# Performance work log

Measured on AMD Instinct MI355X. Metric: run time of the kernel, lower is better.

Reference implementation:

```python
import jax, jax.numpy as jnp
import numpy as np

B, L, D, H = 8, 1024, 1024, 16
DH = D // H  # 64


def setup_inputs() -> dict:
    key = jax.random.key(0)
    ks = jax.random.split(key, 6)
    x = jax.random.normal(ks[0], (B, L, D), dtype=jnp.float32)
    mask = jax.random.randint(ks[1], (1, L, L), 0, 2).astype(jnp.float32)
    # params initialized ~ normal(std=0.1) as in the module's _initialize
    Wk = jax.random.normal(ks[2], (D, D), dtype=jnp.float32) * 0.1
    Wv = jax.random.normal(ks[3], (D, D), dtype=jnp.float32) * 0.1
    Wq = jax.random.normal(ks[4], (D, D), dtype=jnp.float32) * 0.1
    Wo = jax.random.normal(ks[5], (D, D), dtype=jnp.float32) * 0.1
    return {"x": x, "mask": mask, "Wk": Wk, "Wv": Wv, "Wq": Wq, "Wo": Wo}


def reference(x, mask, Wk, Wv, Wq, Wo):
    # torch Linear: y = x @ W.T
    k = jnp.einsum('bld,ed->ble', x, Wk).reshape(B, L, H, DH)
    v = jnp.einsum('bld,ed->ble', x, Wv).reshape(B, L, H, DH)
    q = jnp.einsum('bld,ed->ble', x, Wq).reshape(B, L, H, DH)
    # explicit score matrix [B, H, L, L]
    scores = jnp.einsum('blhe,bmhe->bhlm', q, k)
    m = mask[:, None]  # (1, 1, L, L) broadcasts over batch and heads
    scores = scores * m - 1e9 * (1.0 - m)
    scale = np.float32(1.0 / np.sqrt(DH))
    weights = jax.nn.softmax(scores * scale, axis=-1)
    out = jnp.einsum('bhlm,bmhe->blhe', weights, v).reshape(B, L, D)
    out = jnp.einsum('bld,ed->ble', out, Wo)  # output_linear (n_heads > 1)
    return out
```

## Files before the change

kernel.cpp:

```cpp
#include <hip/hip_runtime.h>

#define B_  8
#define L_  1024
#define D_  1024
#define H_  16
#define DH_ 64

typedef unsigned short u16;
typedef __attribute__((ext_vector_type(8))) short short8;
typedef __attribute__((ext_vector_type(8))) _Float16 half8;
typedef __attribute__((ext_vector_type(4))) float floatx4;
typedef __attribute__((ext_vector_type(16))) float floatx16;

static __device__ __forceinline__ u16 f2bf(float f) {
  union { float f; unsigned u; } cv; cv.f = f;
  unsigned u = cv.u;
  return (u16)((u + 0x7fffu + ((u >> 16) & 1u)) >> 16);
}
static __device__ __forceinline__ u16 f2h(float f) {
  union { _Float16 h; u16 u; } cv; cv.h = (_Float16)f; return cv.u;
}
static __device__ __forceinline__ unsigned pack_bf2(float a, float b) {
  union { float f; unsigned u; } ua, ub; ua.f = a; ub.f = b;
  return __builtin_amdgcn_perm(ub.u + 0x8000u, ua.u + 0x8000u, 0x07060302u);
}

#if __has_builtin(__builtin_amdgcn_exp2f)
#define EXP2(x) __builtin_amdgcn_exp2f(x)
#else
#define EXP2(x) __expf((x) * 0.6931471805599453f)
#endif

__global__ void cast_all(const float* __restrict__ x,  const float* __restrict__ wq,
                         const float* __restrict__ wk, const float* __restrict__ wv,
                         const float* __restrict__ wo, const float* __restrict__ mask,
                         u16* __restrict__ xf,  u16* __restrict__ wqf,
                         u16* __restrict__ wkf, u16* __restrict__ wvf,
                         u16* __restrict__ wof, float* __restrict__ biasP) {
  int blk = blockIdx.x;
  if (blk >= 12288) {
    int i = (blk - 12288) * 256 + threadIdx.x;
    int e = i & 3, lane = (i >> 2) & 63, rr = (i >> 8) & 3, t = (i >> 10) & 1;
    int c = (i >> 11) & 15, w = (i >> 15) & 3, qt = i >> 17;
    int kk  = e + 8 * rr + 4 * (lane >> 5);
    int row = qt * 128 + w * 32 + (lane & 31);
    int key = c * 64 + t * 32 + kk;
    biasP[i] = (mask[(size_t)row * L_ + key] - 1.0f) * 1.8033688e8f - 34.624681f;
    return;
  }
  const float* src; u16* dst; int off;
  if (blk < 8192)       { src = x;  dst = xf;  off = blk; }
  else if (blk < 9216)  { src = wq; dst = wqf; off = blk - 8192; }
  else if (blk < 10240) { src = wk; dst = wkf; off = blk - 9216; }
  else if (blk < 11264) { src = wv; dst = wvf; off = blk - 10240; }
  else                  { src = wo; dst = wof; off = blk - 11264; }
  int i = off * 1024 + threadIdx.x * 4;
  float4 f = *(const float4*)(src + i);
  ushort4 r;
  r.x = f2h(f.x); r.y = f2h(f.y); r.z = f2h(f.z); r.w = f2h(f.w);
  *(ushort4*)(dst + i) = r;
}

typedef __attribute__((address_space(3))) void  lds_void;
typedef const __attribute__((address_space(1))) void g_void;
static __device__ __forceinline__ void load_lds16(const void* g, void* l) {
  __builtin_amdgcn_global_load_lds((g_void*)g, (lds_void*)l, 16, 0, 0);
}

__global__ __launch_bounds__(256) void gemm_qkv(const u16* __restrict__ A,
                                                const u16* __restrict__ wq,
                                                const u16* __restrict__ wk,
                                                const u16* __restrict__ wv,
                                                u16* __restrict__ qf,
                                                u16* __restrict__ kf,
                                                u16* __restrict__ vb) {
  const int K = D_, N = D_;
  int nb = blockIdx.x;
  const u16* Bw; u16* Cp; float scale; int obf;
  if (nb < 8)       { Bw = wq; Cp = qf; scale = 0.18033688f; obf = 0; }
  else if (nb < 16) { Bw = wk; Cp = kf; scale = 1.0f;        obf = 0; }
  else              { Bw = wv; Cp = vb; scale = 1.0f;        obf = 1; }
  const int n0 = (nb & 7) * 128;

  __shared__ u16 lA[2 * 128 * 32];
  __shared__ u16 lB[2 * 128 * 32];
  const int tid  = threadIdx.x;
  const int w    = tid >> 6;
  const int lane = tid & 63;
  const int m    = lane & 15;
  const int kg   = lane >> 4;
  const int m0   = blockIdx.y * 128;
  const int wm   = (w >> 1) * 64;
  const int wn   = (w & 1) * 64;
  const int rowS = tid >> 2;
  const int part = tid & 3;
  const int csrc8 = ((part ^ ((rowS >> 1) & 3))) * 8;
  const int kgs   = (kg ^ ((m >> 1) & 3)) * 8;

  floatx4 acc[4][4];
#pragma unroll
  for (int i = 0; i < 4; ++i)
#pragma unroll
    for (int j = 0; j < 4; ++j)
#pragma unroll
      for (int r = 0; r < 4; ++r) acc[i][j][r] = 0.0f;

  auto STAGE = [&](int k0, int bufsel) {
#pragma unroll
    for (int rnd = 0; rnd < 2; ++rnd) {
      const u16* ga = A  + (size_t)(m0 + rnd * 64 + rowS) * K + k0 + csrc8;
      const u16* gb = Bw + (size_t)(n0 + rnd * 64 + rowS) * K + k0 + csrc8;
      load_lds16(ga, lA + bufsel * 4096 + rnd * 2048 + w * 512);
      load_lds16(gb, lB + bufsel * 4096 + rnd * 2048 + w * 512);
    }
  };

  STAGE(0, 0);
  STAGE(32, 1);

  for (int k0 = 0; k0 < K; k0 += 32) {
    const int buf = (k0 >> 5) & 1;
    if (k0 + 32 < K) { asm volatile("s_waitcnt vmcnt(4)" ::: "memory"); }
    else             { asm volatile("s_waitcnt vmcnt(0)" ::: "memory"); }
    __builtin_amdgcn_s_barrier();
    __builtin_amdgcn_sched_barrier(0);

    const u16* pA = lA + buf * 4096;
    const u16* pB = lB + buf * 4096;
    half8 af[4], bf[4];
#pragma unroll
    for (int i = 0; i < 4; ++i) af[i] = *(const half8*)&pA[(wm + i * 16 + m) * 32 + kgs];
#pragma unroll
    for (int i = 0; i < 4; ++i) bf[i] = *(const half8*)&pB[(wn + i * 16 + m) * 32 + kgs];
#pragma unroll
    for (int mi = 0; mi < 4; ++mi)
#pragma unroll
      for (int ni = 0; ni < 4; ++ni)
        acc[mi][ni] = __builtin_amdgcn_mfma_f32_16x16x32_f16(af[mi], bf[ni], acc[mi][ni], 0, 0, 0);

    __builtin_amdgcn_sched_barrier(0);
    __builtin_amdgcn_s_barrier();
    if (k0 + 64 < K) STAGE(k0 + 64, buf);
  }

#pragma unroll
  for (int mi = 0; mi < 4; ++mi)
#pragma unroll
    for (int ni = 0; ni < 4; ++ni)
#pragma unroll
      for (int r = 0; r < 4; ++r) {
        int row = m0 + wm + mi * 16 + kg * 4 + r;
        int col = n0 + wn + ni * 16 + m;
        size_t idx = (size_t)row * N + col;
        float vv = acc[mi][ni][r] * scale;
        Cp[idx] = obf ? f2bf(vv) : f2h(vv);
      }
}

__global__ __launch_bounds__(256) void gemm_fin(const u16* __restrict__ A,
                                                const u16* __restrict__ Bw,
                                                float* __restrict__ Cp,
                                                int M, int N, int K) {
  __shared__ u16 lA[2 * 128 * 32];
  __shared__ u16 lB[2 * 128 * 32];
  const int tid  = threadIdx.x;
  const int w    = tid >> 6;
  const int lane = tid & 63;
  const int m    = lane & 15;
  const int kg   = lane >> 4;
  const int m0   = blockIdx.y * 128;
  const int n0   = blockIdx.x * 128;
  const int wm   = (w >> 1) * 64;
  const int wn   = (w & 1) * 64;
  const int rowS = tid >> 2;
  const int part = tid & 3;
  const int csrc8 = ((part ^ ((rowS >> 1) & 3))) * 8;
  const int kgs   = (kg ^ ((m >> 1) & 3)) * 8;

  floatx4 acc[4][4];
#pragma unroll
  for (int i = 0; i < 4; ++i)
#pragma unroll
    for (int j = 0; j < 4; ++j)
#pragma unroll
      for (int r = 0; r < 4; ++r) acc[i][j][r] = 0.0f;

  auto STAGE = [&](int k0, int bufsel) {
#pragma unroll
    for (int rnd = 0; rnd < 2; ++rnd) {
      const u16* ga = A  + (size_t)(m0 + rnd * 64 + rowS) * K + k0 + csrc8;
      const u16* gb = Bw + (size_t)(n0 + rnd * 64 + rowS) * K + k0 + csrc8;
      load_lds16(ga, lA + bufsel * 4096 + rnd * 2048 + w * 512);
      load_lds16(gb, lB + bufsel * 4096 + rnd * 2048 + w * 512);
    }
  };

  STAGE(0, 0);
  STAGE(32, 1);

  for (int k0 = 0; k0 < K; k0 += 32) {
    const int buf = (k0 >> 5) & 1;
    if (k0 + 32 < K) { asm volatile("s_waitcnt vmcnt(4)" ::: "memory"); }
    else             { asm volatile("s_waitcnt vmcnt(0)" ::: "memory"); }
    __builtin_amdgcn_s_barrier();
    __builtin_amdgcn_sched_barrier(0);

    const u16* pA = lA + buf * 4096;
    const u16* pB = lB + buf * 4096;
    half8 af[4], bf[4];
#pragma unroll
    for (int i = 0; i < 4; ++i) af[i] = *(const half8*)&pA[(wm + i * 16 + m) * 32 + kgs];
#pragma unroll
    for (int i = 0; i < 4; ++i) bf[i] = *(const half8*)&pB[(wn + i * 16 + m) * 32 + kgs];
#pragma unroll
    for (int mi = 0; mi < 4; ++mi)
#pragma unroll
      for (int ni = 0; ni < 4; ++ni)
        acc[mi][ni] = __builtin_amdgcn_mfma_f32_16x16x32_f16(af[mi], bf[ni], acc[mi][ni], 0, 0, 0);

    __builtin_amdgcn_sched_barrier(0);
    __builtin_amdgcn_s_barrier();
    if (k0 + 64 < K) STAGE(k0 + 64, buf);
  }

#pragma unroll
  for (int mi = 0; mi < 4; ++mi)
#pragma unroll
    for (int ni = 0; ni < 4; ++ni)
#pragma unroll
      for (int r = 0; r < 4; ++r) {
        int row = m0 + wm + mi * 16 + kg * 4 + r;
        int col = n0 + wn + ni * 16 + m;
        Cp[(size_t)row * N + col] = acc[mi][ni][r];
      }
}

__global__ __launch_bounds__(256) void transpose_v(const u16* __restrict__ v,
                                                   u16* __restrict__ vt) {
  __shared__ u16 lds[64][72];
  const int b  = blockIdx.y >> 4;
  const int h  = blockIdx.y & 15;
  const int l0 = blockIdx.x * 64;
  const int tid = threadIdx.x;
#pragma unroll
  for (int it = 0; it < 2; ++it) {
    int idx = it * 256 + tid;
    int i = idx >> 3, off = (idx & 7) * 8;
    *(short8*)&lds[i][off] =
        *(const short8*)(v + ((size_t)(b * L_ + l0 + i)) * D_ + h * 64 + off);
  }
  __syncthreads();
  const int j  = tid >> 2;
  const int p0 = (tid & 3) * 16;
  __attribute__((aligned(16))) u16 tmp[16];
#pragma unroll
  for (int s = 0; s < 16; ++s) {
    int p = p0 + s;
    int l = (p >> 1) + ((p & 1) << 5);
    tmp[s] = lds[l][j];
  }
  u16* dst = vt + ((size_t)((b * H_ + h) * DH_ + j)) * L_ + l0 + p0;
  *(short8*)(dst)     = *(const short8*)&tmp[0];
  *(short8*)(dst + 8) = *(const short8*)&tmp[8];
}

__global__ __launch_bounds__(256, 4) void attn_kernel(const u16* __restrict__ q,
                                                      const u16* __restrict__ k,
                                                      const u16* __restrict__ vt,
                                                      const float* __restrict__ biasP,
                                                      u16* __restrict__ o) {
  __shared__ u16 lK[64][72];
  __shared__ u16 lVt[64][72];
  __shared__ float lRS[4][32];

  const int bh = blockIdx.x, qt = blockIdx.y;
  const int b = bh >> 4, h = bh & 15;
  const int tid = threadIdx.x;
  const int w = tid >> 6, lane = tid & 63;
  const int c32 = lane & 31, hi = lane >> 5;
  const int qr0 = qt * 128 + w * 32;

  const int srow  = tid >> 3;
  const int skoff = (tid & 7) * 8;

  const size_t qbase = ((size_t)((b * L_ + qr0 + c32) * H_ + h)) * DH_;
  half8 aq[4];
#pragma unroll
  for (int ks = 0; ks < 4; ++ks)
    aq[ks] = *(const half8*)(q + qbase + ks * 16 + hi * 8);

  floatx16 acc0, acc1;
#pragma unroll
  for (int i = 0; i < 16; ++i) { acc0[i] = 0.0f; acc1[i] = 0.0f; }
  float rsum0 = 0.0f, rsum1 = 0.0f;

  const u16* kp = k  + ((size_t)((b * L_ + srow) * H_ + h)) * DH_ + skoff;
  const u16* vp = vt + ((size_t)((b * H_ + h) * DH_ + srow)) * L_ + skoff;

  short8 rk[2], rv[2];
#pragma unroll
  for (int it = 0; it < 2; ++it) {
    rk[it] = *(const short8*)(kp + (size_t)it * 32 * H_ * DH_);
    rv[it] = *(const short8*)(vp + (size_t)it * 32 * L_);
  }

  const float4* bp = (const float4*)(biasP + ((size_t)(qt * 4 + w) * 16) * 2048) + lane;

  for (int c = 0; c < 16; ++c) {
    __syncthreads();
#pragma unroll
    for (int it = 0; it < 2; ++it) {
      *(short8*)&lK[it * 32 + srow][skoff]  = rk[it];
      *(short8*)&lVt[it * 32 + srow][skoff] = rv[it];
    }
    __syncthreads();

    floatx16 s0, s1;
#pragma unroll
    for (int rr = 0; rr < 4; ++rr) {
      float4 b0 = bp[rr * 64];
      float4 b1 = bp[(4 + rr) * 64];
      s0[rr * 4 + 0] = b0.x; s0[rr * 4 + 1] = b0.y; s0[rr * 4 + 2] = b0.z; s0[rr * 4 + 3] = b0.w;
      s1[rr * 4 + 0] = b1.x; s1[rr * 4 + 1] = b1.y; s1[rr * 4 + 2] = b1.z; s1[rr * 4 + 3] = b1.w;
    }
    bp += 512;

    if (c < 15) {
      kp += (size_t)64 * H_ * DH_;
      vp += 64;
#pragma unroll
      for (int it = 0; it < 2; ++it) {
        rk[it] = *(const short8*)(kp + (size_t)it * 32 * H_ * DH_);
        rv[it] = *(const short8*)(vp + (size_t)it * 32 * L_);
      }
    }

#pragma unroll
    for (int ks = 0; ks < 4; ++ks) {
      half8 bk0 = *(const half8*)&lK[c32][ks * 16 + hi * 8];
      half8 bk1 = *(const half8*)&lK[32 + c32][ks * 16 + hi * 8];
      s0 = __builtin_amdgcn_mfma_f32_32x32x16_f16(bk0, aq[ks], s0, 0, 0, 0);
      s1 = __builtin_amdgcn_mfma_f32_32x32x16_f16(bk1, aq[ks], s1, 0, 0, 0);
    }

    union { short8 v[4]; unsigned u[16]; } ap;
#pragma unroll
    for (int reg = 0; reg < 16; ++reg) {
      float p0 = EXP2(s0[reg]);
      float p1 = EXP2(s1[reg]);
      ap.u[reg] = pack_bf2(p0, p1);
      if (reg & 1) rsum1 += p0 + p1; else rsum0 += p0 + p1;
    }

#pragma unroll
    for (int ks = 0; ks < 4; ++ks) {
      short8 bv0 = *(const short8*)&lVt[c32][ks * 16 + hi * 8];
      short8 bv1 = *(const short8*)&lVt[32 + c32][ks * 16 + hi * 8];
      acc0 = __builtin_amdgcn_mfma_f32_32x32x16_bf16(ap.v[ks], bv0, acc0, 0, 0, 0);
      acc1 = __builtin_amdgcn_mfma_f32_32x32x16_bf16(ap.v[ks], bv1, acc1, 0, 0, 0);
    }
  }

  float rsum = rsum0 + rsum1;
  rsum += __shfl_xor(rsum, 32, 64);
  if (hi == 0) lRS[w][c32] = rsum;

#pragma unroll
  for (int reg = 0; reg < 16; ++reg) {
    int rl = (reg & 3) + 8 * (reg >> 2) + 4 * hi;
    float inv = 1.0f / lRS[w][rl];
    int row = qr0 + rl;
    size_t obase = ((size_t)((b * L_ + row) * H_ + h)) * DH_;
    o[obase + c32]      = f2h(acc0[reg] * inv);
    o[obase + 32 + c32] = f2h(acc1[reg] * inv);
  }
}

extern "C" void kernel_launch(void* const* d_in, const int* in_sizes, int n_in,
                              void* d_out, int out_size, void* d_ws, size_t ws_size,
                              hipStream_t stream) {
  const float* x    = (const float*)d_in[0];
  const float* mask = (const float*)d_in[1];
  const float* Wk   = (const float*)d_in[2];
  const float* Wv   = (const float*)d_in[3];
  const float* Wq   = (const float*)d_in[4];
  const float* Wo   = (const float*)d_in[5];

  char* ws = (char*)d_ws;
  u16* xf    = (u16*)(ws);
  u16* aout  = xf;
  u16* kf    = (u16*)(ws + (16ull << 20));
  u16* vtb   = (u16*)(ws + (32ull << 20));
  float* biasP = (float*)(ws + (48ull << 20));
  u16* wqf   = (u16*)(ws + (52ull << 20));
  u16* wkf   = (u16*)(ws + (54ull << 20));
  u16* wvf   = (u16*)(ws + (56ull << 20));
  u16* wof   = (u16*)(ws + (58ull << 20));
  u16* qf = (u16*)d_out;
  u16* vb = qf + (size_t)B_ * L_ * D_;

  cast_all<<<16384, 256, 0, stream>>>(x, Wq, Wk, Wv, Wo, mask,
                                      xf, wqf, wkf, wvf, wof, biasP);

  gemm_qkv<<<dim3(24, 64), 256, 0, stream>>>(xf, wqf, wkf, wvf, qf, kf, vb);

  transpose_v<<<dim3(L_ / 64, B_ * H_), 256, 0, stream>>>(vb, vtb);

  attn_kernel<<<dim3(B_ * H_, L_ / 128), 256, 0, stream>>>(qf, kf, vtb, biasP, aout);

  gemm_fin<<<dim3(D_ / 128, (B_ * L_) / 128), 256, 0, stream>>>(
      aout, wof, (float*)d_out, B_ * L_, D_, D_);
}
```

Before: 255.1 us.

## Restructure QKV GEMM to 256x256 tiles with 4-stage LDS pipeline

Rewrites the fused QKV projection GEMM to use 512-thread blocks computing 256x256 output tiles, replacing the previous 128x128 tiles with 256 threads. It adds a four-buffer LDS ring that interleaves global-to-LDS loads with the two halves of the MFMA work, uses setprio around the MFMA bursts, and remaps block indices with a swizzle for L2 locality. The larger tiles raise data reuse per LDS load and cut global traffic, at the cost of more registers, more shared memory, and fewer blocks (384), which may hurt occupancy and wave balance.

New measurement: 254.0 us. Within noise of the previous version (-0.4%).

```diff
diff --git a/kernel.cpp b/kernel.cpp
--- a/kernel.cpp
+++ b/kernel.cpp
@@ -67,93 +67,134 @@
   __builtin_amdgcn_global_load_lds((g_void*)g, (lds_void*)l, 16, 0, 0);
 }
 
-__global__ __launch_bounds__(256) void gemm_qkv(const u16* __restrict__ A,
-                                                const u16* __restrict__ wq,
-                                                const u16* __restrict__ wk,
-                                                const u16* __restrict__ wv,
-                                                u16* __restrict__ qf,
-                                                u16* __restrict__ kf,
-                                                u16* __restrict__ vb) {
-  const int K = D_, N = D_;
-  int nb = blockIdx.x;
+__global__ __launch_bounds__(512, 2) void gemm_qkv(const u16* __restrict__ A,
+                                                   const u16* __restrict__ wq,
+                                                   const u16* __restrict__ wk,
+                                                   const u16* __restrict__ wv,
+                                                   u16* __restrict__ qf,
+                                                   u16* __restrict__ kf,
+                                                   u16* __restrict__ vb) {
+  const int K = D_;
+  __shared__ u16 lA4[4 * 8192];
+  __shared__ u16 lB4[4 * 8192];
+
+  int flat = blockIdx.y * 12 + blockIdx.x;
+  int swz  = (flat & 7) * 48 + (flat >> 3);
+  int nb   = swz % 12;
+  int mb   = swz / 12;
+
   const u16* Bw; u16* Cp; float scale; int obf;
-  if (nb < 8)       { Bw = wq; Cp = qf; scale = 0.18033688f; obf = 0; }
-  else if (nb < 16) { Bw = wk; Cp = kf; scale = 1.0f;        obf = 0; }
-  else              { Bw = wv; Cp = vb; scale = 1.0f;        obf = 1; }
-  const int n0 = (nb & 7) * 128;
-
-  __shared__ u16 lA[2 * 128 * 32];
-  __shared__ u16 lB[2 * 128 * 32];
+  int wsel = nb >> 2;
+  if (wsel == 0)      { Bw = wq; Cp = qf; scale = 0.18033688f; obf = 0; }
+  else if (wsel == 1) { Bw = wk; Cp = kf; scale = 1.0f;        obf = 0; }
+  else                { Bw = wv; Cp = vb; scale = 1.0f;        obf = 1; }
+  const int m0g = mb * 256;
+  const int n0w = (nb & 3) * 256;
+
   const int tid  = threadIdx.x;
-  const int w    = tid >> 6;
+  const int wid  = tid >> 6;
   const int lane = tid & 63;
-  const int m    = lane & 15;
+  const int m16  = lane & 15;
   const int kg   = lane >> 4;
-  const int m0   = blockIdx.y * 128;
-  const int wm   = (w >> 1) * 64;
-  const int wn   = (w & 1) * 64;
-  const int rowS = tid >> 2;
-  const int part = tid & 3;
-  const int csrc8 = ((part ^ ((rowS >> 1) & 3))) * 8;
-  const int kgs   = (kg ^ ((m >> 1) & 3)) * 8;
-
-  floatx4 acc[4][4];
-#pragma unroll
-  for (int i = 0; i < 4; ++i)
+  const int xorv = m16 & 7;
+  const int wm   = wid >> 2;
+  const int wn   = wid & 3;
+
+  const int ldaBase = m16 * 64 + (((wm * 4 + kg) ^ xorv) * 8);
+  const int ldbBase = ((wn & 1) * 64 + m16) * 64 + ((((wn >> 1) * 4 + kg) ^ xorv) * 8);
+
+  const int cl0 = tid,       rho0 = cl0 >> 3;
+  const int c0  = (cl0 & 7) ^ (rho0 & 7);
+  const int mr0 = rho0 + ((c0 >> 2) << 7), kb0 = c0 & 3;
+  const int cl1 = 512 + tid, rho1 = cl1 >> 3;
+  const int c1  = (cl1 & 7) ^ (rho1 & 7);
+  const int mr1 = rho1 + ((c1 >> 2) << 7), kb1 = c1 & 3;
+
+  const u16* srcA0 = A  + (size_t)(m0g + mr0) * K + kb0 * 8;
+  const u16* srcA1 = A  + (size_t)(m0g + mr1) * K + kb1 * 8;
+  const u16* srcB0 = Bw + (size_t)(n0w + mr0) * K + kb0 * 8;
+  const u16* srcB1 = Bw + (size_t)(n0w + mr1) * K + kb1 * 8;
+  const int dst0 = wid * 512;
+  const int dst1 = 4096 + wid * 512;
+
+  floatx4 acc[8][4];
+#pragma unroll
+  for (int i = 0; i < 8; ++i)
 #pragma unroll
     for (int j = 0; j < 4; ++j)
 #pragma unroll
       for (int r = 0; r < 4; ++r) acc[i][j][r] = 0.0f;
 
-  auto STAGE = [&](int k0, int bufsel) {
-#pragma unroll
-    for (int rnd = 0; rnd < 2; ++rnd) {
-      const u16* ga = A  + (size_t)(m0 + rnd * 64 + rowS) * K + k0 + csrc8;
-      const u16* gb = Bw + (size_t)(n0 + rnd * 64 + rowS) * K + k0 + csrc8;
-      load_lds16(ga, lA + bufsel * 4096 + rnd * 2048 + w * 512);
-      load_lds16(gb, lB + bufsel * 4096 + rnd * 2048 + w * 512);
-    }
+  load_lds16(srcA0, lA4 + 0 * 8192 + dst0);
+  load_lds16(srcB0, lB4 + 0 * 8192 + dst0);
+  load_lds16(srcA1, lA4 + 0 * 8192 + dst1);
+  load_lds16(srcB1, lB4 + 0 * 8192 + dst1);
+  load_lds16(srcA0 + 32, lA4 + 1 * 8192 + dst0);
+  load_lds16(srcB0 + 32, lB4 + 1 * 8192 + dst0);
+  load_lds16(srcA1 + 32, lA4 + 1 * 8192 + dst1);
+  load_lds16(srcB1 + 32, lB4 + 1 * 8192 + dst1);
+  asm volatile("s_waitcnt vmcnt(4)" ::: "memory");
+  __builtin_amdgcn_s_barrier();
+
+  auto TILE = [&](int t, int buf) {
+    const u16* bA = lA4 + buf * 8192;
+    const u16* bB = lB4 + buf * 8192;
+    const int t2 = t + 2;
+    const int kk = t2 * 32;
+    half8 af[8], bf[4];
+#pragma unroll
+    for (int i = 0; i < 4; ++i) af[i] = *(const half8*)&bA[ldaBase + i * 1024];
+#pragma unroll
+    for (int i = 0; i < 4; ++i) bf[i] = *(const half8*)&bB[ldbBase + i * 1024];
+    if (t2 < 32) {
+      load_lds16(srcA0 + kk, lA4 + (t2 & 3) * 8192 + dst0);
+      load_lds16(srcB0 + kk, lB4 + (t2 & 3) * 8192 + dst0);
+    }
+    __builtin_amdgcn_s_barrier();
+    __builtin_amdgcn_s_setprio(1);
+#pragma unroll
+    for (int i = 0; i < 4; ++i)
+#pragma unroll
+      for (int j = 0; j < 4; ++j)
+        acc[i][j] = __builtin_amdgcn_mfma_f32_16x16x32_f16(af[i], bf[j], acc[i][j], 0, 0, 0);
+    __builtin_amdgcn_s_setprio(0);
+    __builtin_amdgcn_s_barrier();
+#pragma unroll
+    for (int i = 4; i < 8; ++i) af[i] = *(const half8*)&bA[ldaBase + i * 1024];
+    if (t2 < 32) {
+      load_lds16(srcA1 + kk, lA4 + (t2 & 3) * 8192 + dst1);
+      load_lds16(srcB1 + kk, lB4 + (t2 & 3) * 8192 + dst1);
+    }
+    __builtin_amdgcn_s_barrier();
+    __builtin_amdgcn_s_setprio(1);
+#pragma unroll
+    for (int i = 4; i < 8; ++i)
+#pragma unroll
+      for (int j = 0; j < 4; ++j)
+        acc[i][j] = __builtin_amdgcn_mfma_f32_16x16x32_f16(af[i], bf[j], acc[i][j], 0, 0, 0);
+    __builtin_amdgcn_s_setprio(0);
+    if (t < 30)       asm volatile("s_waitcnt vmcnt(4)" ::: "memory");
+    else if (t == 30) asm volatile("s_waitcnt vmcnt(0)" ::: "memory");
+    __builtin_amdgcn_s_barrier();
   };
 
-  STAGE(0, 0);
-  STAGE(32, 1);
-
-  for (int k0 = 0; k0 < K; k0 += 32) {
-    const int buf = (k0 >> 5) & 1;
-    if (k0 + 32 < K) { asm volatile("s_waitcnt vmcnt(4)" ::: "memory"); }
-    else             { asm volatile("s_waitcnt vmcnt(0)" ::: "memory"); }
-    __builtin_amdgcn_s_barrier();
-    __builtin_amdgcn_sched_barrier(0);
-
-    const u16* pA = lA + buf * 4096;
-    const u16* pB = lB + buf * 4096;
-    half8 af[4], bf[4];
-#pragma unroll
-    for (int i = 0; i < 4; ++i) af[i] = *(const half8*)&pA[(wm + i * 16 + m) * 32 + kgs];
-#pragma unroll
-    for (int i = 0; i < 4; ++i) bf[i] = *(const half8*)&pB[(wn + i * 16 + m) * 32 + kgs];
-#pragma unroll
-    for (int mi = 0; mi < 4; ++mi)
-#pragma unroll
-      for (int ni = 0; ni < 4; ++ni)
-        acc[mi][ni] = __builtin_amdgcn_mfma_f32_16x16x32_f16(af[mi], bf[ni], acc[mi][ni], 0, 0, 0);
-
-    __builtin_amdgcn_sched_barrier(0);
-    __builtin_amdgcn_s_barrier();
-    if (k0 + 64 < K) STAGE(k0 + 64, buf);
-  }
-
-#pragma unroll
-  for (int mi = 0; mi < 4; ++mi)
-#pragma unroll
-    for (int ni = 0; ni < 4; ++ni)
+  for (int tt = 0; tt < 32; tt += 4) {
+    TILE(tt + 0, 0);
+    TILE(tt + 1, 1);
+    TILE(tt + 2, 2);
+    TILE(tt + 3, 3);
+  }
+
+#pragma unroll
+  for (int fm = 0; fm < 8; ++fm)
+#pragma unroll
+    for (int fn = 0; fn < 4; ++fn)
 #pragma unroll
       for (int r = 0; r < 4; ++r) {
-        int row = m0 + wm + mi * 16 + kg * 4 + r;
-        int col = n0 + wn + ni * 16 + m;
-        size_t idx = (size_t)row * N + col;
-        float vv = acc[mi][ni][r] * scale;
-        Cp[idx] = obf ? f2bf(vv) : f2h(vv);
+        int row = m0g + wm * 128 + fm * 16 + kg * 4 + r;
+        int col = (nb & 3) * 256 + wn * 64 + fn * 16 + m16;
+        float vv = acc[fm][fn][r] * scale;
+        Cp[(size_t)row * D_ + col] = obf ? f2bf(vv) : f2h(vv);
       }
 }
 
@@ -402,7 +443,7 @@
   cast_all<<<16384, 256, 0, stream>>>(x, Wq, Wk, Wv, Wo, mask,
                                       xf, wqf, wkf, wvf, wof, biasP);
 
-  gemm_qkv<<<dim3(24, 64), 256, 0, stream>>>(xf, wqf, wkf, wvf, qf, kf, vb);
+  gemm_qkv<<<dim3(12, 32), 512, 0, stream>>>(xf, wqf, wkf, wvf, qf, kf, vb);
 
   transpose_v<<<dim3(L_ / 64, B_ * H_), 256, 0, stream>>>(vb, vtb);
 
```

## Double-buffer K/V tiles in LDS to halve per-iteration barriers

Applied to the files above, without the earlier changes.

The attention kernel now keeps two LDS buffers for the K and V^T tiles. The next tile's registers are written into the alternate buffer while the current one is consumed, so only one __syncthreads per iteration is needed instead of two. Global prefetch now runs two tiles ahead. In exchange, LDS use per block doubles, which may limit occupancy at the launch bound of 4 blocks per CU, and more registers stay live.

New measurement: 257.2 us. Within noise of the previous version (+0.8%).

```diff
diff --git a/kernel.cpp b/kernel.cpp
--- a/kernel.cpp
+++ b/kernel.cpp
@@ -269,8 +269,8 @@
                                                       const u16* __restrict__ vt,
                                                       const float* __restrict__ biasP,
                                                       u16* __restrict__ o) {
-  __shared__ u16 lK[64][72];
-  __shared__ u16 lVt[64][72];
+  __shared__ u16 lK[2][64][72];
+  __shared__ u16 lVt[2][64][72];
   __shared__ float lRS[4][32];
 
   const int bh = blockIdx.x, qt = blockIdx.y;
@@ -303,17 +303,40 @@
     rk[it] = *(const short8*)(kp + (size_t)it * 32 * H_ * DH_);
     rv[it] = *(const short8*)(vp + (size_t)it * 32 * L_);
   }
+#pragma unroll
+  for (int it = 0; it < 2; ++it) {
+    *(short8*)&lK[0][it * 32 + srow][skoff]  = rk[it];
+    *(short8*)&lVt[0][it * 32 + srow][skoff] = rv[it];
+  }
+  kp += (size_t)64 * H_ * DH_;
+  vp += 64;
+#pragma unroll
+  for (int it = 0; it < 2; ++it) {
+    rk[it] = *(const short8*)(kp + (size_t)it * 32 * H_ * DH_);
+    rv[it] = *(const short8*)(vp + (size_t)it * 32 * L_);
+  }
+  __syncthreads();
 
   const float4* bp = (const float4*)(biasP + ((size_t)(qt * 4 + w) * 16) * 2048) + lane;
 
   for (int c = 0; c < 16; ++c) {
-    __syncthreads();
-#pragma unroll
-    for (int it = 0; it < 2; ++it) {
-      *(short8*)&lK[it * 32 + srow][skoff]  = rk[it];
-      *(short8*)&lVt[it * 32 + srow][skoff] = rv[it];
-    }
-    __syncthreads();
+    const int buf = c & 1;
+    if (c < 15) {
+#pragma unroll
+      for (int it = 0; it < 2; ++it) {
+        *(short8*)&lK[buf ^ 1][it * 32 + srow][skoff]  = rk[it];
+        *(short8*)&lVt[buf ^ 1][it * 32 + srow][skoff] = rv[it];
+      }
+    }
+    if (c < 14) {
+      kp += (size_t)64 * H_ * DH_;
+      vp += 64;
+#pragma unroll
+      for (int it = 0; it < 2; ++it) {
+        rk[it] = *(const short8*)(kp + (size_t)it * 32 * H_ * DH_);
+        rv[it] = *(const short8*)(vp + (size_t)it * 32 * L_);
+      }
+    }
 
     floatx16 s0, s1;
 #pragma unroll
@@ -325,20 +348,10 @@
     }
     bp += 512;
 
-    if (c < 15) {
-      kp += (size_t)64 * H_ * DH_;
-      vp += 64;
-#pragma unroll
-      for (int it = 0; it < 2; ++it) {
-        rk[it] = *(const short8*)(kp + (size_t)it * 32 * H_ * DH_);
-        rv[it] = *(const short8*)(vp + (size_t)it * 32 * L_);
-      }
-    }
-
 #pragma unroll
     for (int ks = 0; ks < 4; ++ks) {
-      half8 bk0 = *(const half8*)&lK[c32][ks * 16 + hi * 8];
-      half8 bk1 = *(const half8*)&lK[32 + c32][ks * 16 + hi * 8];
+      half8 bk0 = *(const half8*)&lK[buf][c32][ks * 16 + hi * 8];
+      half8 bk1 = *(const half8*)&lK[buf][32 + c32][ks * 16 + hi * 8];
       s0 = __builtin_amdgcn_mfma_f32_32x32x16_f16(bk0, aq[ks], s0, 0, 0, 0);
       s1 = __builtin_amdgcn_mfma_f32_32x32x16_f16(bk1, aq[ks], s1, 0, 0, 0);
     }
@@ -354,11 +367,13 @@
 
 #pragma unroll
     for (int ks = 0; ks < 4; ++ks) {
-      short8 bv0 = *(const short8*)&lVt[c32][ks * 16 + hi * 8];
-      short8 bv1 = *(const short8*)&lVt[32 + c32][ks * 16 + hi * 8];
+      short8 bv0 = *(const short8*)&lVt[buf][c32][ks * 16 + hi * 8];
+      short8 bv1 = *(const short8*)&lVt[buf][32 + c32][ks * 16 + hi * 8];
       acc0 = __builtin_amdgcn_mfma_f32_32x32x16_bf16(ap.v[ks], bv0, acc0, 0, 0, 0);
       acc1 = __builtin_amdgcn_mfma_f32_32x32x16_bf16(ap.v[ks], bv1, acc1, 0, 0, 0);
     }
+
+    __syncthreads();
   }
 
   float rsum = rsum0 + rsum1;
```
